# Kernel tuning notes

Measured on AMD Instinct MI355X. Metric: run time of the kernel, lower is better.

Reference implementation:

```python
import jax, jax.numpy as jnp
import numpy as np

B, S, D, F, UNITS = 32, 128, 32, 32, 11
NEG = -1.0e9


def setup_inputs() -> dict:
    key = jax.random.key(0)
    ks = jax.random.split(key, 8)
    X = jax.random.normal(ks[0], (B, S, D), dtype=jnp.float32)
    V = jax.random.normal(ks[1], (B, S, F), dtype=jnp.float32)
    # Dense(units) params (glorot-ish scale)
    sc = 1.0 / np.sqrt(D)
    W1 = jax.random.normal(ks[2], (D, UNITS), dtype=jnp.float32) * sc
    W2 = jax.random.normal(ks[3], (D, UNITS), dtype=jnp.float32) * sc
    W3 = jax.random.normal(ks[4], (D, UNITS), dtype=jnp.float32) * sc
    b1 = jnp.zeros((UNITS,), jnp.float32)
    b2 = jnp.zeros((UNITS,), jnp.float32)
    b3 = jnp.zeros((UNITS,), jnp.float32)
    return {"X": X, "V": V, "W1": W1, "b1": b1, "W2": W2, "b2": b2, "W3": W3, "b3": b3}


def reference(X, V, W1, b1, W2, b2, W3, b3):
    b, s, _ = X.shape
    # mask=None path: only the diagonal additive mask
    a = jnp.eye(s, dtype=X.dtype) * NEG  # [S,S]
    Q1 = X @ W1 + b1  # [B,S,U]
    Q2 = X @ W2 + b2
    Q3 = X @ W3 + b3
    A = jnp.einsum('biu,bju->bij', Q1, Q2) + a  # dot1 core
    Bm = jnp.einsum('bju,bku->bjk', Q2, Q3) + a  # dot2 core
    C = jnp.einsum('biu,bku->bik', Q1, Q3) + a  # dot3 core
    # threeway scores [B,S,S,S]
    scores = (A[:, :, :, None] + Bm[:, None, :, :] + C[:, :, None, :]) / 9.0
    # joint softmax over axes (1,2,3)
    p = jax.nn.softmax(scores.reshape(b, -1), axis=-1).reshape(b, s, s, s)
    # sum_{ijk} p_ijk * concat(V_i, V_j, V_k) = concat(m1@V, m2@V, m3@V)
    m1 = p.sum(axis=(2, 3))  # [B,S] marginal over i
    m2 = p.sum(axis=(1, 3))  # marginal over j
    m3 = p.sum(axis=(1, 2))  # marginal over k
    out1 = jnp.einsum('bs,bsf->bf', m1, V)
    out2 = jnp.einsum('bs,bsf->bf', m2, V)
    out3 = jnp.einsum('bs,bsf->bf', m3, V)
    return jnp.concatenate([out1, out2, out3], axis=-1)  # [B,3F]
```

## Files before the change

### kernel.cpp

```cpp
#include <hip/hip_runtime.h>
#include <hip/hip_bf16.h>


#define B_ 32
#define S_ 128
#define D_ 32
#define F_ 32
#define U_ 11
#define INV9 (1.0f / 9.0f)

__global__ __launch_bounds__(256) void k_qe(const float* __restrict__ X,
    const float* __restrict__ W1, const float* __restrict__ b1,
    const float* __restrict__ W2, const float* __restrict__ b2,
    const float* __restrict__ W3, const float* __restrict__ b3,
    float* __restrict__ E) {
    int blk = blockIdx.x;
    int b = blk / 12;
    int rest = blk - b * 12;
    int m = rest >> 2;
    int tl = rest & 3;
    __shared__ float Xs[S_][D_ + 1];
    __shared__ float QR[S_][13];
    __shared__ float QL[32][13];
    __shared__ float Ws[2][D_][U_];
    __shared__ float bsh[2][U_];
    int t = threadIdx.x;

    const float* Xb = X + (size_t)b * S_ * D_;
    for (int idx = t; idx < S_ * D_; idx += 256) Xs[idx >> 5][idx & 31] = Xb[idx];
    const float* WL = (m == 0) ? W1 : (m == 1) ? W2 : W1;
    const float* WR = (m == 0) ? W2 : (m == 1) ? W3 : W3;
    const float* bL = (m == 0) ? b1 : (m == 1) ? b2 : b1;
    const float* bR = (m == 0) ? b2 : (m == 1) ? b3 : b3;
    for (int idx = t; idx < D_ * U_; idx += 256) {
        Ws[0][idx / U_][idx % U_] = WL[idx];
        Ws[1][idx / U_][idx % U_] = WR[idx];
    }
    if (t < U_) { bsh[0][t] = bL[t]; bsh[1][t] = bR[t]; }
    __syncthreads();

    if (t < 160) {
        int isR = (t < 128);
        int side = isR ? 1 : 0;
        int row = isR ? t : (tl * 32 + (t - 128));
        float q[U_];
#pragma unroll
        for (int u = 0; u < U_; ++u) q[u] = bsh[side][u];
#pragma unroll
        for (int d = 0; d < D_; ++d) {
            float x = Xs[row][d];
#pragma unroll
            for (int u = 0; u < U_; ++u) q[u] += x * Ws[side][d][u];
        }
        float* dst = isR ? &QR[t][0] : &QL[t - 128][0];
#pragma unroll
        for (int u = 0; u < U_; ++u) dst[u] = q[u];
    }
    __syncthreads();

    float* Eb = E + (size_t)(b * 3 + m) * (S_ * S_);
    for (int idx = t; idx < 32 * S_; idx += 256) {
        int il = idx >> 7, j = idx & 127;
        int i = tl * 32 + il;
        float s = 0.f;
#pragma unroll
        for (int u = 0; u < U_; ++u) s += QL[il][u] * QR[j][u];
        Eb[i * S_ + j] = (i == j) ? 0.f : __expf(s * INV9);
    }
}

__global__ __launch_bounds__(256, 4) void k_marg(const float* __restrict__ E,
    float* __restrict__ m1p, float* __restrict__ m2p, float* __restrict__ m3p) {
    int bid = blockIdx.x;
    int b   = bid & 31;
    int job = (bid >> 5) & 1;
    int cc  = (bid >> 6) & 7;
    int kh  = bid >> 9;
    int c0  = cc * 16, kk0 = kh * 64;
    const float* EA = E + (size_t)b * 3 * S_ * S_;
    const float* EB = EA + S_ * S_;
    const float* EC = EB + S_ * S_;
    const float* Bsrc = job ? EC : EB;
    const float* Wsrc = job ? EB : EC;

    __shared__ float At[16][132];
    __shared__ float Bs[16][68];
    float* red = &At[0][0];

    int t = threadIdx.x;

    if (job == 0) {
#pragma unroll
        for (int q = 0; q < 2; ++q) {
            int idx = t + q * 256;
            int i = idx >> 2;
            int j4 = (idx & 3) * 4;
            float4 v = *(const float4*)&EA[(size_t)i * S_ + c0 + j4];
            At[j4 + 0][i] = v.x; At[j4 + 1][i] = v.y;
            At[j4 + 2][i] = v.z; At[j4 + 3][i] = v.w;
        }
    } else {
#pragma unroll
        for (int q = 0; q < 2; ++q) {
            int idx = t + q * 256;
            int cl = idx >> 5;
            int col4 = (idx & 31) * 4;
            *(float4*)&At[cl][col4] =
                *(const float4*)&EA[(size_t)(c0 + cl) * S_ + col4];
        }
    }
    {
        int cl = t >> 4;
        int k4 = (t & 15) * 4;
        *(float4*)&Bs[cl][k4] =
            *(const float4*)&Bsrc[(size_t)(c0 + cl) * S_ + kk0 + k4];
    }
    __syncthreads();

    int r0 = (t >> 4) * 8;
    int k0 = (t & 15) * 4;
    float acc[8][4] = {};
#pragma unroll
    for (int c = 0; c < 16; ++c) {
        float4 a0 = *(const float4*)&At[c][r0];
        float4 a1 = *(const float4*)&At[c][r0 + 4];
        float4 bv = *(const float4*)&Bs[c][k0];
        float av[8] = {a0.x, a0.y, a0.z, a0.w, a1.x, a1.y, a1.z, a1.w};
#pragma unroll
        for (int x = 0; x < 8; ++x) {
            acc[x][0] += av[x] * bv.x; acc[x][1] += av[x] * bv.y;
            acc[x][2] += av[x] * bv.z; acc[x][3] += av[x] * bv.w;
        }
    }

    float rs[8], cs[4] = {0.f, 0.f, 0.f, 0.f};
#pragma unroll
    for (int x = 0; x < 8; ++x) {
        float4 w = *(const float4*)&Wsrc[(size_t)(r0 + x) * S_ + kk0 + k0];
        float v0 = w.x * acc[x][0], v1 = w.y * acc[x][1];
        float v2 = w.z * acc[x][2], v3 = w.w * acc[x][3];
        rs[x] = v0 + v1 + v2 + v3;
        cs[0] += v0; cs[1] += v1; cs[2] += v2; cs[3] += v3;
    }
#pragma unroll
    for (int x = 0; x < 8; ++x) {
        rs[x] += __shfl_xor(rs[x], 1);
        rs[x] += __shfl_xor(rs[x], 2);
        rs[x] += __shfl_xor(rs[x], 4);
        rs[x] += __shfl_xor(rs[x], 8);
    }
    if ((t & 15) == 0) {
        float* MO = job ? m2p : m1p;
        size_t base = ((size_t)b * 16 + cc * 2 + kh) * S_ + r0;
#pragma unroll
        for (int x = 0; x < 8; ++x) MO[base + x] = rs[x];
    }
    if (!job) {
#pragma unroll
        for (int y = 0; y < 4; ++y) {
            cs[y] += __shfl_xor(cs[y], 16);
            cs[y] += __shfl_xor(cs[y], 32);
        }
        __syncthreads();
        if ((t & 63) < 16) {
            int w = t >> 6;
            *(float4*)&red[w * 64 + k0] = make_float4(cs[0], cs[1], cs[2], cs[3]);
        }
        __syncthreads();
        if (t < 64)
            m3p[((size_t)b * 8 + cc) * S_ + kk0 + t] =
                red[t] + red[64 + t] + red[128 + t] + red[192 + t];
    }
}

__global__ __launch_bounds__(128) void k_out(const float* __restrict__ m1p,
    const float* __restrict__ m2p, const float* __restrict__ m3p,
    const float* __restrict__ V, float* __restrict__ out) {
    int b = blockIdx.x, t = threadIdx.x;
    __shared__ float ms[3][S_];
    __shared__ float Vs[S_][33];
    __shared__ float zr[2];
    const float* Vb = V + (size_t)b * S_ * F_;
#pragma unroll
    for (int q = 0; q < 8; ++q) {
        int idx = t + q * 128;
        int row = idx >> 3, c4 = (idx & 7) * 4;
        float4 v = *(const float4*)&Vb[row * F_ + c4];
        Vs[row][c4 + 0] = v.x; Vs[row][c4 + 1] = v.y;
        Vs[row][c4 + 2] = v.z; Vs[row][c4 + 3] = v.w;
    }
    size_t b16 = (size_t)b * 16 * S_ + t;
    float v1 = 0.f, v2 = 0.f;
#pragma unroll
    for (int p = 0; p < 16; ++p) {
        v1 += m1p[b16 + p * S_];
        v2 += m2p[b16 + p * S_];
    }
    size_t b8 = (size_t)b * 8 * S_ + t;
    float v3 = 0.f;
#pragma unroll
    for (int p = 0; p < 8; ++p) v3 += m3p[b8 + p * S_];
    ms[0][t] = v1; ms[1][t] = v2; ms[2][t] = v3;
    float z = v1;
#pragma unroll
    for (int off = 32; off; off >>= 1) z += __shfl_xor(z, off);
    if ((t & 63) == 0) zr[t >> 6] = z;
    __syncthreads();
    float invZ = 1.0f / (zr[0] + zr[1]);
    if (t < 96) {
        int which = t >> 5, f = t & 31;
        const float* ml = &ms[which][0];
        float s = 0.f;
#pragma unroll 8
        for (int s0 = 0; s0 < S_; ++s0) s += ml[s0] * Vs[s0][f];
        out[(size_t)b * 96 + t] = s * invZ;
    }
}

extern "C" void kernel_launch(void* const* d_in, const int* in_sizes, int n_in,
                              void* d_out, int out_size, void* d_ws, size_t ws_size,
                              hipStream_t stream) {
    const float* X  = (const float*)d_in[0];
    const float* V  = (const float*)d_in[1];
    const float* W1 = (const float*)d_in[2];
    const float* b1 = (const float*)d_in[3];
    const float* W2 = (const float*)d_in[4];
    const float* b2 = (const float*)d_in[5];
    const float* W3 = (const float*)d_in[6];
    const float* b3 = (const float*)d_in[7];
    float* out = (float*)d_out;

    float* E   = (float*)d_ws;
    float* m1p = E + (size_t)B_ * 3 * S_ * S_;
    float* m2p = m1p + (size_t)B_ * 16 * S_;
    float* m3p = m2p + (size_t)B_ * 16 * S_;

    k_qe<<<B_ * 12, 256, 0, stream>>>(X, W1, b1, W2, b2, W3, b3, E);
    k_marg<<<1024, 256, 0, stream>>>(E, m1p, m2p, m3p);
    k_out<<<B_, 128, 0, stream>>>(m1p, m2p, m3p, V, out);
}
```

Baseline: 23.95 us.

## Fuse output reduction into marginal kernel via last-block atomic counter

Removes the separate k_out launch. Each k_marg block increments a per-batch atomic counter after a threadfence, and the last block for each batch reduces the partial marginals and computes the output against V. The counters are zeroed in the first kernel. This saves a kernel launch and its gap, at the cost of an atomic and a fence per block and a serialized tail block per batch.

```diff
diff --git a/kernel.cpp b/kernel.cpp
--- a/kernel.cpp
+++ b/kernel.cpp
@@ -13,7 +13,7 @@
     const float* __restrict__ W1, const float* __restrict__ b1,
     const float* __restrict__ W2, const float* __restrict__ b2,
     const float* __restrict__ W3, const float* __restrict__ b3,
-    float* __restrict__ E) {
+    float* __restrict__ E, unsigned int* __restrict__ cnt) {
     int blk = blockIdx.x;
     int b = blk / 12;
     int rest = blk - b * 12;
@@ -26,6 +26,8 @@
     __shared__ float bsh[2][U_];
     int t = threadIdx.x;
 
+    if (blk < 32 && t == 0) cnt[blk] = 0;
+
     const float* Xb = X + (size_t)b * S_ * D_;
     for (int idx = t; idx < S_ * D_; idx += 256) Xs[idx >> 5][idx & 31] = Xb[idx];
     const float* WL = (m == 0) ? W1 : (m == 1) ? W2 : W1;
@@ -70,22 +72,26 @@
 }
 
 __global__ __launch_bounds__(256, 4) void k_marg(const float* __restrict__ E,
-    float* __restrict__ m1p, float* __restrict__ m2p, float* __restrict__ m3p) {
+    float* __restrict__ m1p, float* __restrict__ m2p, float* __restrict__ m3p,
+    const float* __restrict__ V, float* __restrict__ out,
+    unsigned int* __restrict__ cnt) {
     int bid = blockIdx.x;
     int b   = bid & 31;
     int job = (bid >> 5) & 1;
     int cc  = (bid >> 6) & 7;
     int kh  = bid >> 9;
     int c0  = cc * 16, kk0 = kh * 64;
-    const float* EA = E + (size_t)b * 3 * S_ * S_;
-    const float* EB = EA + S_ * S_;
-    const float* EC = EB + S_ * S_;
-    const float* Bsrc = job ? EC : EB;
-    const float* Wsrc = job ? EB : EC;
-
-    __shared__ float At[16][132];
-    __shared__ float Bs[16][68];
-    float* red = &At[0][0];
+    const float* EA  = E + (size_t)b * 3 * S_ * S_;
+    const float* EBm = EA + S_ * S_;
+    const float* ECm = EBm + S_ * S_;
+    const float* Bsrc = job ? ECm : EBm;
+    const float* Wsrc = job ? EBm : ECm;
+
+    __shared__ __align__(16) float pool[4624];
+    __shared__ unsigned int lastflag;
+    float* At = pool;
+    float* Bs = pool + 2112;
+    float* red = pool;
 
     int t = threadIdx.x;
 
@@ -93,11 +99,11 @@
 #pragma unroll
         for (int q = 0; q < 2; ++q) {
             int idx = t + q * 256;
-            int i = idx >> 2;
-            int j4 = (idx & 3) * 4;
-            float4 v = *(const float4*)&EA[(size_t)i * S_ + c0 + j4];
-            At[j4 + 0][i] = v.x; At[j4 + 1][i] = v.y;
-            At[j4 + 2][i] = v.z; At[j4 + 3][i] = v.w;
+            int i  = idx >> 2;
+            int jj = (idx & 3) * 4;
+            float4 v = *(const float4*)&EA[(size_t)i * S_ + c0 + jj];
+            At[(jj + 0) * 132 + i] = v.x; At[(jj + 1) * 132 + i] = v.y;
+            At[(jj + 2) * 132 + i] = v.z; At[(jj + 3) * 132 + i] = v.w;
         }
     } else {
 #pragma unroll
@@ -105,14 +111,14 @@
             int idx = t + q * 256;
             int cl = idx >> 5;
             int col4 = (idx & 31) * 4;
-            *(float4*)&At[cl][col4] =
+            *(float4*)&At[cl * 132 + col4] =
                 *(const float4*)&EA[(size_t)(c0 + cl) * S_ + col4];
         }
     }
     {
         int cl = t >> 4;
         int k4 = (t & 15) * 4;
-        *(float4*)&Bs[cl][k4] =
+        *(float4*)&Bs[cl * 68 + k4] =
             *(const float4*)&Bsrc[(size_t)(c0 + cl) * S_ + kk0 + k4];
     }
     __syncthreads();
@@ -122,9 +128,9 @@
     float acc[8][4] = {};
 #pragma unroll
     for (int c = 0; c < 16; ++c) {
-        float4 a0 = *(const float4*)&At[c][r0];
-        float4 a1 = *(const float4*)&At[c][r0 + 4];
-        float4 bv = *(const float4*)&Bs[c][k0];
+        float4 a0 = *(const float4*)&At[c * 132 + r0];
+        float4 a1 = *(const float4*)&At[c * 132 + r0 + 4];
+        float4 bv = *(const float4*)&Bs[c * 68 + k0];
         float av[8] = {a0.x, a0.y, a0.z, a0.w, a1.x, a1.y, a1.z, a1.w};
 #pragma unroll
         for (int x = 0; x < 8; ++x) {
@@ -171,49 +177,54 @@
             m3p[((size_t)b * 8 + cc) * S_ + kk0 + t] =
                 red[t] + red[64 + t] + red[128 + t] + red[192 + t];
     }
-}
-
-__global__ __launch_bounds__(128) void k_out(const float* __restrict__ m1p,
-    const float* __restrict__ m2p, const float* __restrict__ m3p,
-    const float* __restrict__ V, float* __restrict__ out) {
-    int b = blockIdx.x, t = threadIdx.x;
-    __shared__ float ms[3][S_];
-    __shared__ float Vs[S_][33];
-    __shared__ float zr[2];
-    const float* Vb = V + (size_t)b * S_ * F_;
-#pragma unroll
-    for (int q = 0; q < 8; ++q) {
-        int idx = t + q * 128;
-        int row = idx >> 3, c4 = (idx & 7) * 4;
-        float4 v = *(const float4*)&Vb[row * F_ + c4];
-        Vs[row][c4 + 0] = v.x; Vs[row][c4 + 1] = v.y;
-        Vs[row][c4 + 2] = v.z; Vs[row][c4 + 3] = v.w;
-    }
-    size_t b16 = (size_t)b * 16 * S_ + t;
-    float v1 = 0.f, v2 = 0.f;
-#pragma unroll
-    for (int p = 0; p < 16; ++p) {
-        v1 += m1p[b16 + p * S_];
-        v2 += m2p[b16 + p * S_];
-    }
-    size_t b8 = (size_t)b * 8 * S_ + t;
-    float v3 = 0.f;
-#pragma unroll
-    for (int p = 0; p < 8; ++p) v3 += m3p[b8 + p * S_];
-    ms[0][t] = v1; ms[1][t] = v2; ms[2][t] = v3;
-    float z = v1;
-#pragma unroll
-    for (int off = 32; off; off >>= 1) z += __shfl_xor(z, off);
-    if ((t & 63) == 0) zr[t >> 6] = z;
-    __syncthreads();
-    float invZ = 1.0f / (zr[0] + zr[1]);
-    if (t < 96) {
-        int which = t >> 5, f = t & 31;
-        const float* ml = &ms[which][0];
-        float s = 0.f;
+
+    __syncthreads();
+    __threadfence();
+    if (t == 0) lastflag = (atomicAdd(&cnt[b], 1u) == 31u) ? 1u : 0u;
+    __syncthreads();
+    if (lastflag) {
+        __threadfence();
+        float* Vs = pool;
+        float* ms = pool + 4224;
+        float* zr = pool + 4608;
+        __syncthreads();
+        const float* Vb = V + (size_t)b * S_ * F_;
+#pragma unroll
+        for (int q = 0; q < 4; ++q) {
+            int idx = t + q * 256;
+            int row = idx >> 3, c4 = (idx & 7) * 4;
+            float4 v = *(const float4*)&Vb[row * F_ + c4];
+            Vs[row * 33 + c4 + 0] = v.x; Vs[row * 33 + c4 + 1] = v.y;
+            Vs[row * 33 + c4 + 2] = v.z; Vs[row * 33 + c4 + 3] = v.w;
+        }
+        float v1 = 0.f;
+        if (t < S_) {
+            size_t b16 = (size_t)b * 16 * S_ + t;
+            float v2 = 0.f, v3 = 0.f;
+#pragma unroll
+            for (int p = 0; p < 16; ++p) {
+                v1 += m1p[b16 + p * S_];
+                v2 += m2p[b16 + p * S_];
+            }
+            size_t b8 = (size_t)b * 8 * S_ + t;
+#pragma unroll
+            for (int p = 0; p < 8; ++p) v3 += m3p[b8 + p * S_];
+            ms[t] = v1; ms[S_ + t] = v2; ms[2 * S_ + t] = v3;
+        }
+        float z = v1;
+#pragma unroll
+        for (int off = 32; off; off >>= 1) z += __shfl_xor(z, off);
+        if ((t & 63) == 0) zr[t >> 6] = z;
+        __syncthreads();
+        float invZ = 1.0f / (zr[0] + zr[1] + zr[2] + zr[3]);
+        if (t < 96) {
+            int which = t >> 5, f = t & 31;
+            const float* ml = &ms[which * S_];
+            float s = 0.f;
 #pragma unroll 8
-        for (int s0 = 0; s0 < S_; ++s0) s += ml[s0] * Vs[s0][f];
-        out[(size_t)b * 96 + t] = s * invZ;
+            for (int s0 = 0; s0 < S_; ++s0) s += ml[s0] * Vs[s0 * 33 + f];
+            out[(size_t)b * 96 + t] = s * invZ;
+        }
     }
 }
 
@@ -234,8 +245,8 @@
     float* m1p = E + (size_t)B_ * 3 * S_ * S_;
     float* m2p = m1p + (size_t)B_ * 16 * S_;
     float* m3p = m2p + (size_t)B_ * 16 * S_;
-
-    k_qe<<<B_ * 12, 256, 0, stream>>>(X, W1, b1, W2, b2, W3, b3, E);
-    k_marg<<<1024, 256, 0, stream>>>(E, m1p, m2p, m3p);
-    k_out<<<B_, 128, 0, stream>>>(m1p, m2p, m3p, V, out);
+    unsigned int* cnt = (unsigned int*)(m3p + (size_t)B_ * 8 * S_);
+
+    k_qe<<<B_ * 12, 256, 0, stream>>>(X, W1, b1, W2, b2, W3, b3, E, cnt);
+    k_marg<<<1024, 256, 0, stream>>>(E, m1p, m2p, m3p, V, out, cnt);
 }
```

Result: slower. 90.07 us (+276.0%).
